# Performance work log

Measured on AMD Instinct MI355X. Metric: run time of the kernel, lower is better.

The kernel has to match this reference:

```python
import jax, jax.numpy as jnp
import numpy as np

B, T, H = 2, 2048, 2048
QH, KH, D = 16, 8, 128
F = 8192
EPS = 1e-06
MASK_VALUE = -1e30


def _rms_norm(x, gamma, eps=EPS):
    rms = jnp.sqrt(jnp.mean(x.astype(jnp.float32) ** 2, axis=-1, keepdims=True) + eps)
    return (gamma * x / rms).astype(jnp.bfloat16)


def _rope(x, sin, cos):
    # x: [B,T,h,D]; sin/cos: [B,T,D//2]
    x1, x2 = x[..., : x.shape[-1] // 2], x[..., x.shape[-1] // 2:]
    s, c = sin[:, :, None, :], cos[:, :, None, :]
    return jnp.concatenate([x1 * c - x2 * s, x2 * c + x1 * s], axis=-1)


def _attention(q, k, v, q_idx, k_idx, q_pos, k_pos):
    # q: [B,QH,T,D]; k,v: [B,KH,T,D]. Online-softmax tiling in the original is
    # mathematically identical to a single stable softmax over the full causal row.
    orig = q.dtype
    q = q.astype(jnp.float32)
    k = k.astype(jnp.float32)
    v = v.astype(jnp.float32)
    rep = q.shape[1] // k.shape[1]
    k = jnp.repeat(k, rep, axis=1)
    v = jnp.repeat(v, rep, axis=1)
    scale = 1.0 / jnp.sqrt(jnp.asarray(q.shape[-1], jnp.float32))
    s = jnp.einsum('bhqd,bhkd->bhqk', q, k) * scale
    mask = (q_idx[:, None, :, None] & k_idx[:, None, None, :]) & (
        q_pos[:, None, :, None] >= k_pos[:, None, None, :])
    s = jnp.where(mask, s, MASK_VALUE)
    p = jax.nn.softmax(s, axis=-1)
    o = jnp.einsum('bhqk,bhkd->bhqd', p, v)
    return o.astype(orig)


def _block(x, sin, cos, token_mask, pre_gamma, wq, wk, wv, q_gamma, k_gamma, wo,
           post_gamma, wg, wu, wd):
    bf = jnp.bfloat16
    Bx, Tx = x.shape[0], x.shape[1]
    x_norm = _rms_norm(x, pre_gamma)                     # bf16
    q = (x_norm @ wq.astype(bf)).reshape(Bx, Tx, QH, D)
    k = (x_norm @ wk.astype(bf)).reshape(Bx, Tx, KH, D)
    v = (x_norm @ wv.astype(bf)).reshape(Bx, Tx, KH, D)
    q = _rope(_rms_norm(q, q_gamma), sin, cos)           # promotes to f32 (matches flax)
    k = _rope(_rms_norm(k, k_gamma), sin, cos)
    idx = token_mask != 0
    pos = jax.lax.broadcasted_iota(jnp.int32, token_mask.shape, 1)
    attn = _attention(q.swapaxes(1, 2), k.swapaxes(1, 2), v.swapaxes(1, 2),
                      idx, idx, pos, pos)
    attn = attn.swapaxes(1, 2).reshape(Bx, Tx, QH * D)
    x = x + attn.astype(bf) @ wo.astype(bf)
    x_norm = _rms_norm(x, post_gamma)
    g = jax.nn.silu(x_norm @ wg.astype(bf))
    y = g * (x_norm @ wu.astype(bf))
    x = x + y @ wd.astype(bf)
    return x, k, v


def setup_inputs() -> dict:
    key = jax.random.key(0)
    ks = jax.random.split(key, 8)

    def w(kk, shape):
        return jax.random.normal(kk, shape, jnp.float32) * 0.02

    x = jax.random.normal(ks[0], (B, T, H), jnp.float32)
    pos = jnp.arange(T, dtype=jnp.float32)
    inv_freq = 1.0 / (10000.0 ** (jnp.arange(D // 2, dtype=jnp.float32) / (D // 2)))
    ang = pos[:, None] * inv_freq[None, :]
    sin = jnp.broadcast_to(jnp.sin(ang)[None], (B, T, D // 2))
    cos = jnp.broadcast_to(jnp.cos(ang)[None], (B, T, D // 2))
    return {
        'x': x, 'sin': sin, 'cos': cos,
        'token_mask': jnp.ones((B, T), jnp.int32),
        'layer_id': 0,
        'pre_gamma': jnp.ones((H,), jnp.float32),
        'wq': w(ks[1], (H, QH * D)),
        'wk': w(ks[2], (H, KH * D)),
        'wv': w(ks[3], (H, KH * D)),
        'q_gamma': jnp.ones((D,), jnp.float32),
        'k_gamma': jnp.ones((D,), jnp.float32),
        'wo': w(ks[4], (QH * D, H)),
        'post_gamma': jnp.ones((H,), jnp.float32),
        'wg': w(ks[5], (H, F)),
        'wu': w(ks[6], (H, F)),
        'wd': w(ks[7], (F, H)),
    }


def reference(x, sin, cos, token_mask, layer_id, pre_gamma, wq, wk, wv, q_gamma,
              k_gamma, wo, post_gamma, wg, wu, wd):
    # cache=None path: layer_id is unused.
    return _block(x, sin, cos, token_mask, pre_gamma, wq, wk, wv, q_gamma,
                  k_gamma, wo, post_gamma, wg, wu, wd)
```

## Files before the change

kernel.cpp:

```cpp
#include <hip/hip_runtime.h>
#include <hip/hip_bf16.h>


#define Bc  2
#define Tc  2048
#define Hc  2048
#define QHc 16
#define KHc 8
#define Dc  128
#define Fc  8192
#define Mc  (Bc*Tc)
#define FCHUNK 2048
#define EPSc 1e-6f
#define MASKVAL (-1e30f)

typedef __bf16  bf16x8 __attribute__((ext_vector_type(8)));
typedef short   short8 __attribute__((ext_vector_type(8)));
typedef float   f32x4  __attribute__((ext_vector_type(4)));

__device__ __forceinline__ float waveReduceSum(float v) {
    for (int off = 32; off > 0; off >>= 1) v += __shfl_down(v, off, 64);
    return v;
}

__device__ __forceinline__ void load_lds_16(const __hip_bfloat16* g,
                                            __hip_bfloat16* l) {
    __builtin_amdgcn_global_load_lds(
        (const __attribute__((address_space(1))) void*)g,
        (__attribute__((address_space(3))) void*)l, 16, 0, 0);
}

__global__ __launch_bounds__(256) void rmsnorm_f32_kernel(
    const float* __restrict__ in, const float* __restrict__ gamma,
    __hip_bfloat16* __restrict__ out, int width)
{
    const int row = blockIdx.x;
    const float* r = in + (size_t)row * width;
    float ss = 0.f;
    for (int i = threadIdx.x; i < width; i += 256) { float v = r[i]; ss += v * v; }
    ss = waveReduceSum(ss);
    __shared__ float red[4];
    if ((threadIdx.x & 63) == 0) red[threadIdx.x >> 6] = ss;
    __syncthreads();
    const float tot = red[0] + red[1] + red[2] + red[3];
    const float inv = 1.0f / sqrtf(tot / (float)width + EPSc);
    __hip_bfloat16* o = out + (size_t)row * width;
    for (int i = threadIdx.x; i < width; i += 256)
        o[i] = __float2bfloat16(gamma[i] * r[i] * inv);
}

__global__ __launch_bounds__(128) void qknorm_rope_kernel(
    const __hip_bfloat16* in, const float* __restrict__ gamma,
    const float* __restrict__ sinp, const float* __restrict__ cosp,
    __hip_bfloat16* outB, float* outF, int heads)
{
    const int row = blockIdx.x;
    const int bt  = row / heads;
    const int d   = threadIdx.x;
    const float v = __bfloat162float(in[(size_t)row * Dc + d]);
    float ss = waveReduceSum(v * v);
    __shared__ float red[2];
    __shared__ float nrm[Dc];
    if ((d & 63) == 0) red[d >> 6] = ss;
    __syncthreads();
    const float rms = sqrtf((red[0] + red[1]) * (1.0f / (float)Dc) + EPSc);
    const float xn = __bfloat162float(__float2bfloat16(gamma[d] * v / rms));
    nrm[d] = xn;
    __syncthreads();
    float res;
    if (d < 64) {
        const float s = sinp[(size_t)bt * 64 + d];
        const float c = cosp[(size_t)bt * 64 + d];
        res = nrm[d] * c - nrm[d + 64] * s;
    } else {
        const float s = sinp[(size_t)bt * 64 + (d - 64)];
        const float c = cosp[(size_t)bt * 64 + (d - 64)];
        res = nrm[d] * c + nrm[d - 64] * s;
    }
    outB[(size_t)row * Dc + d] = __float2bfloat16(res);
    if (outF) outF[(size_t)row * Dc + d] = res;
}

__global__ __launch_bounds__(256) void convert_transpose_kernel(
    const float* __restrict__ W, __hip_bfloat16* __restrict__ Wt, int K, int N)
{
    __shared__ float tile[32][33];
    const int tx = threadIdx.x & 31;
    const int ty = threadIdx.x >> 5;
    const int n0 = blockIdx.x * 32;
    const int k0 = blockIdx.y * 32;
    for (int r = 0; r < 4; ++r) {
        const int k = ty + r * 8;
        tile[k][tx] = W[(size_t)(k0 + k) * N + n0 + tx];
    }
    __syncthreads();
    for (int r = 0; r < 4; ++r) {
        const int n = ty + r * 8;
        Wt[(size_t)(n0 + n) * K + k0 + tx] = __float2bfloat16(tile[tx][n]);
    }
}


__device__ __forceinline__ void stage_unitA256(
    const __hip_bfloat16* __restrict__ Ag, __hip_bfloat16* bufBase,
    int m0, int lda, int kk0, int h, int tid)
{
#pragma unroll
    for (int p = 0; p < 2; ++p) {
        const int ci = p * 512 + tid;
        const int rl = ci >> 3;
        const int cc = ci & 7;
        const int grow = m0 + ((rl >> 6) * 128) + h * 64 + (rl & 63);
        const int scc = cc ^ (rl & 7);
        load_lds_16(Ag + (size_t)grow * lda + kk0 + scc * 8,
                    bufBase + h * 8192 + ci * 8);
    }
}

__device__ __forceinline__ void stage_unitB256(
    const __hip_bfloat16* __restrict__ Bg, __hip_bfloat16* bufBase,
    int n0, int ldt, int kk0, int h, int tid)
{
#pragma unroll
    for (int p = 0; p < 2; ++p) {
        const int ci = p * 512 + tid;
        const int rl = ci >> 3;
        const int cc = ci & 7;
        const int grow = n0 + h * 128 + rl;
        const int scc = cc ^ (rl & 7);
        load_lds_16(Bg + (size_t)grow * ldt + kk0 + scc * 8,
                    bufBase + h * 8192 + ci * 8);
    }
}

__device__ __forceinline__ bf16x8 read_frag256(const __hip_bfloat16* buf,
                                               int r, int w)
{
    const int cc = w ^ (r & 7);
    return *reinterpret_cast<const bf16x8*>(buf + r * 64 + cc * 8);
}

template <int MODE>
__global__ __launch_bounds__(512, 2) void gemm256_kernel(
    const __hip_bfloat16* __restrict__ A, const __hip_bfloat16* __restrict__ Bt,
    __hip_bfloat16* outB, float* outF, const float* resid,
    const __hip_bfloat16* gmul, int M, int N, int K, int lda, int ldt, int ldc)
{
    __shared__ __hip_bfloat16 smem[65536];
    __hip_bfloat16* Ab0 = smem;
    __hip_bfloat16* Ab1 = smem + 16384;
    __hip_bfloat16* Bb0 = smem + 32768;
    __hip_bfloat16* Bb1 = smem + 49152;

    const int tid  = threadIdx.x;
    const int lane = tid & 63;
    const int wave = tid >> 6;
    const int l15  = lane & 15;
    const int quad = lane >> 4;
    const int wm   = wave >> 2;
    const int wn   = wave & 3;
    const int m0   = blockIdx.y * 256;
    const int n0   = blockIdx.x * 256;
    const int NTt  = K >> 6;

    f32x4 acc[8][4];
    const f32x4 zero = {0.f, 0.f, 0.f, 0.f};
#pragma unroll
    for (int i = 0; i < 8; ++i)
#pragma unroll
        for (int j = 0; j < 4; ++j) acc[i][j] = zero;

    stage_unitA256(A, Ab0, m0, lda, 0, 0, tid);
    stage_unitA256(A, Ab0, m0, lda, 0, 1, tid);
    stage_unitB256(Bt, Bb0, n0, ldt, 0, 0, tid);
    stage_unitB256(Bt, Bb0, n0, ldt, 0, 1, tid);
    if (NTt > 1) {
        stage_unitA256(A, Ab1, m0, lda, 64, 0, tid);
        stage_unitB256(Bt, Bb1, n0, ldt, 64, 0, tid);
        stage_unitB256(Bt, Bb1, n0, ldt, 64, 1, tid);
    }
    asm volatile("s_waitcnt vmcnt(0)" ::: "memory");
    asm volatile("s_barrier" ::: "memory");

    bf16x8 bfr[4][2];
    bf16x8 af[4];

#define GB_READ_B(BB)                                                         \
    _Pragma("unroll")                                                         \
    for (int nt = 0; nt < 4; ++nt) {                                          \
        bfr[nt][0] = read_frag256(BB, wn * 64 + nt * 16 + l15, quad);         \
        bfr[nt][1] = read_frag256(BB, wn * 64 + nt * 16 + l15, 4 + quad);     \
    }
#define GB_READ_A(AB, MG, KS)                                                 \
    _Pragma("unroll")                                                         \
    for (int mq = 0; mq < 4; ++mq)                                            \
        af[mq] = read_frag256(AB, (MG)*128 + wm * 64 + mq * 16 + l15,         \
                              (KS)*4 + quad);
#define GB_MFMA(MG, KS)                                                       \
    __builtin_amdgcn_s_setprio(1);                                            \
    _Pragma("unroll")                                                         \
    for (int nt = 0; nt < 4; ++nt)                                            \
    _Pragma("unroll")                                                         \
    for (int mq = 0; mq < 4; ++mq)                                            \
        acc[(MG)*4 + mq][nt] = __builtin_amdgcn_mfma_f32_16x16x32_bf16(       \
            af[mq], bfr[nt][KS], acc[(MG)*4 + mq][nt], 0, 0, 0);              \
    __builtin_amdgcn_s_setprio(0);
#define SBAR256 asm volatile("s_barrier" ::: "memory")
#define VMC6    asm volatile("s_waitcnt vmcnt(6)" ::: "memory")

    const int nIter = NTt >> 1;
    for (int it = 0; it < nIter; ++it) {
        const int t1 = 2 * it + 1, t2 = 2 * it + 2, t3 = 2 * it + 3;
        GB_READ_B(Bb0); GB_READ_A(Ab0, 0, 0);
        stage_unitA256(A, Ab1, m0, lda, t1 * 64, 1, tid);
        SBAR256; GB_MFMA(0, 0); SBAR256;
        GB_READ_A(Ab0, 0, 1);
        if (t2 < NTt) stage_unitB256(Bt, Bb0, n0, ldt, t2 * 64, 0, tid);
        SBAR256; GB_MFMA(0, 1); SBAR256;
        GB_READ_A(Ab0, 1, 0);
        if (t2 < NTt) stage_unitB256(Bt, Bb0, n0, ldt, t2 * 64, 1, tid);
        SBAR256; GB_MFMA(1, 0); SBAR256;
        GB_READ_A(Ab0, 1, 1);
        if (t2 < NTt) stage_unitA256(A, Ab0, m0, lda, t2 * 64, 0, tid);
        SBAR256; GB_MFMA(1, 1); VMC6; SBAR256;
        GB_READ_B(Bb1); GB_READ_A(Ab1, 0, 0);
        if (t2 < NTt) stage_unitA256(A, Ab0, m0, lda, t2 * 64, 1, tid);
        SBAR256; GB_MFMA(0, 0); SBAR256;
        GB_READ_A(Ab1, 0, 1);
        if (t3 < NTt) stage_unitB256(Bt, Bb1, n0, ldt, t3 * 64, 0, tid);
        SBAR256; GB_MFMA(0, 1); SBAR256;
        GB_READ_A(Ab1, 1, 0);
        if (t3 < NTt) stage_unitB256(Bt, Bb1, n0, ldt, t3 * 64, 1, tid);
        SBAR256; GB_MFMA(1, 0); SBAR256;
        GB_READ_A(Ab1, 1, 1);
        if (t3 < NTt) stage_unitA256(A, Ab1, m0, lda, t3 * 64, 0, tid);
        SBAR256; GB_MFMA(1, 1); VMC6; SBAR256;
    }

#undef GB_READ_B
#undef GB_READ_A
#undef GB_MFMA
#undef SBAR256
#undef VMC6

#pragma unroll
    for (int m = 0; m < 8; ++m) {
#pragma unroll
        for (int nt = 0; nt < 4; ++nt) {
            const f32x4 a  = acc[m][nt];
            const int col  = n0 + wn * 64 + nt * 16 + l15;
            const int rowb = m0 + wm * 128 + (m >> 2) * 64 + (m & 3) * 16 + quad * 4;
#pragma unroll
            for (int r = 0; r < 4; ++r) {
                const size_t idx = (size_t)(rowb + r) * ldc + col;
                const float val = a[r];
                if constexpr (MODE == 0) {
                    outB[idx] = __float2bfloat16(val);
                } else if constexpr (MODE == 1) {
                    outF[idx] = resid[idx] +
                                __bfloat162float(__float2bfloat16(val));
                } else if constexpr (MODE == 3) {
                    const float g = __bfloat162float(gmul[idx]);
                    const float sil = __bfloat162float(
                        __float2bfloat16(g / (1.f + __expf(-g))));
                    const float u = __bfloat162float(__float2bfloat16(val));
                    outB[idx] = __float2bfloat16(sil * u);
                } else {
                    const __hip_bfloat16 b = __float2bfloat16(val);
                    outB[idx] = b;
                    outF[idx] = __bfloat162float(b);
                }
            }
        }
    }
}

template <int MODE>
__global__ __launch_bounds__(256) void gemm_bt_kernel(
    const __hip_bfloat16* __restrict__ A, const __hip_bfloat16* __restrict__ Bt,
    __hip_bfloat16* outB, float* outF, const float* resid,
    const __hip_bfloat16* gmul, int M, int N, int K, int lda, int ldt)
{
    __shared__ __hip_bfloat16 As[128 * 32];
    __shared__ __hip_bfloat16 Bs[128 * 32];

    const int tid  = threadIdx.x;
    const int lane = tid & 63;
    const int wave = tid >> 6;
    const int l15  = lane & 15;
    const int quad = lane >> 4;
    const int q8   = quad * 8;
    const int wm   = wave >> 1;
    const int wn   = wave & 1;
    const int m0   = blockIdx.y * 128;
    const int n0   = blockIdx.x * 128;

    const int c0 = tid, c1 = tid + 256;
    const int r0 = c0 >> 2, o0 = (c0 & 3) * 8;
    const int r1 = c1 >> 2, o1 = (c1 & 3) * 8;
    const __hip_bfloat16* gA0 = A + (size_t)(m0 + r0) * lda + o0;
    const __hip_bfloat16* gA1 = A + (size_t)(m0 + r1) * lda + o1;
    const __hip_bfloat16* gB0 = Bt + (size_t)(n0 + r0) * ldt + o0;
    const __hip_bfloat16* gB1 = Bt + (size_t)(n0 + r1) * ldt + o1;

    f32x4 acc[4][4];
    const f32x4 zero = {0.f, 0.f, 0.f, 0.f};
#pragma unroll
    for (int i = 0; i < 4; ++i)
#pragma unroll
        for (int j = 0; j < 4; ++j) acc[i][j] = zero;

    for (int k0 = 0; k0 < K; k0 += 32) {
        __syncthreads();
        load_lds_16(gA0 + k0, As + c0 * 8);
        load_lds_16(gA1 + k0, As + c1 * 8);
        load_lds_16(gB0 + k0, Bs + c0 * 8);
        load_lds_16(gB1 + k0, Bs + c1 * 8);
        __syncthreads();

        bf16x8 af[4], bfv[4];
#pragma unroll
        for (int mt = 0; mt < 4; ++mt)
            af[mt] = *reinterpret_cast<const bf16x8*>(
                As + (wm * 64 + mt * 16 + l15) * 32 + q8);
#pragma unroll
        for (int nt = 0; nt < 4; ++nt)
            bfv[nt] = *reinterpret_cast<const bf16x8*>(
                Bs + (wn * 64 + nt * 16 + l15) * 32 + q8);
#pragma unroll
        for (int mt = 0; mt < 4; ++mt)
#pragma unroll
            for (int nt = 0; nt < 4; ++nt)
                acc[mt][nt] = __builtin_amdgcn_mfma_f32_16x16x32_bf16(
                    af[mt], bfv[nt], acc[mt][nt], 0, 0, 0);
    }

#pragma unroll
    for (int mt = 0; mt < 4; ++mt) {
#pragma unroll
        for (int nt = 0; nt < 4; ++nt) {
            const f32x4 a  = acc[mt][nt];
            const int col  = n0 + wn * 64 + nt * 16 + l15;
            const int rowb = m0 + wm * 64 + mt * 16 + quad * 4;
#pragma unroll
            for (int r = 0; r < 4; ++r) {
                const size_t idx = (size_t)(rowb + r) * N + col;
                const float val = a[r];
                if constexpr (MODE == 0) {
                    outB[idx] = __float2bfloat16(val);
                } else if constexpr (MODE == 1) {
                    outF[idx] = resid[idx] +
                                __bfloat162float(__float2bfloat16(val));
                } else if constexpr (MODE == 3) {
                    const float g = __bfloat162float(gmul[idx]);
                    const float sil = __bfloat162float(
                        __float2bfloat16(g / (1.f + __expf(-g))));
                    const float u = __bfloat162float(__float2bfloat16(val));
                    outB[idx] = __float2bfloat16(sil * u);
                } else {
                    const __hip_bfloat16 b = __float2bfloat16(val);
                    outB[idx] = b;
                    outF[idx] = __bfloat162float(b);
                }
            }
        }
    }
}

template <int MODE>
__global__ __launch_bounds__(256) void gemm_kernel(
    const __hip_bfloat16* __restrict__ A, const float* __restrict__ Bw,
    __hip_bfloat16* outB, float* outF, const float* resid,
    const __hip_bfloat16* gmul, int M, int N, int K, int ldb)
{
    __shared__ __hip_bfloat16 As[128][32];
    __shared__ __hip_bfloat16 Bs[128][40];

    const int tid  = threadIdx.x;
    const int lane = tid & 63;
    const int wave = tid >> 6;
    const int l15  = lane & 15;
    const int quad = lane >> 4;
    const int q8   = quad * 8;
    const int wm   = wave >> 1;
    const int wn   = wave & 1;
    const int m0   = blockIdx.y * 128;
    const int n0   = blockIdx.x * 128;

    f32x4 acc[4][4];
    const f32x4 zero = {0.f, 0.f, 0.f, 0.f};
#pragma unroll
    for (int i = 0; i < 4; ++i)
#pragma unroll
        for (int j = 0; j < 4; ++j) acc[i][j] = zero;

    const int nK = K >> 5;
    for (int kt = 0; kt < nK; ++kt) {
        const int k0 = kt << 5;
        __syncthreads();
#pragma unroll
        for (int vv = 0; vv < 2; ++vv) {
            const int vi  = vv * 256 + tid;
            const int row = vi >> 2;
            const int col = (vi & 3) * 8;
            *(short8*)(&As[row][col]) =
                *(const short8*)(A + (size_t)(m0 + row) * K + k0 + col);
        }
        {
            const int n  = tid & 127;
            const int kk = tid >> 7;
            const float* bp = Bw + (size_t)k0 * ldb + n0 + n;
#pragma unroll
            for (int p = 0; p < 16; ++p) {
                const int k = p * 2 + kk;
                Bs[n][k] = __float2bfloat16(bp[(size_t)k * ldb]);
            }
        }
        __syncthreads();
        bf16x8 af[4], bfv[4];
#pragma unroll
        for (int mt = 0; mt < 4; ++mt)
            af[mt] = *reinterpret_cast<const bf16x8*>(&As[wm * 64 + mt * 16 + l15][q8]);
#pragma unroll
        for (int nt = 0; nt < 4; ++nt)
            bfv[nt] = *reinterpret_cast<const bf16x8*>(&Bs[wn * 64 + nt * 16 + l15][q8]);
#pragma unroll
        for (int mt = 0; mt < 4; ++mt)
#pragma unroll
            for (int nt = 0; nt < 4; ++nt)
                acc[mt][nt] = __builtin_amdgcn_mfma_f32_16x16x32_bf16(
                    af[mt], bfv[nt], acc[mt][nt], 0, 0, 0);
    }

#pragma unroll
    for (int mt = 0; mt < 4; ++mt) {
#pragma unroll
        for (int nt = 0; nt < 4; ++nt) {
            const f32x4 a  = acc[mt][nt];
            const int col  = n0 + wn * 64 + nt * 16 + l15;
            const int rowb = m0 + wm * 64 + mt * 16 + quad * 4;
#pragma unroll
            for (int r = 0; r < 4; ++r) {
                const size_t idx = (size_t)(rowb + r) * N + col;
                const float val = a[r];
                if constexpr (MODE == 0) {
                    outB[idx] = __float2bfloat16(val);
                } else if constexpr (MODE == 1) {
                    outF[idx] = resid[idx] +
                                __bfloat162float(__float2bfloat16(val));
                } else if constexpr (MODE == 3) {
                    const float g = __bfloat162float(gmul[idx]);
                    const float sil = __bfloat162float(
                        __float2bfloat16(g / (1.f + __expf(-g))));
                    const float u = __bfloat162float(__float2bfloat16(val));
                    outB[idx] = __float2bfloat16(sil * u);
                } else {
                    const __hip_bfloat16 b = __float2bfloat16(val);
                    outB[idx] = b;
                    outF[idx] = __bfloat162float(b);
                }
            }
        }
    }
}

__global__ __launch_bounds__(256) void flash_attn_kernel(
    const __hip_bfloat16* q, const __hip_bfloat16* __restrict__ k,
    const __hip_bfloat16* __restrict__ v, const int* __restrict__ mask,
    __hip_bfloat16* out)
{
    __shared__ unsigned short Ks[64][136];
    __shared__ unsigned short Vs[128][72];
    __shared__ unsigned short Ps[4][16][72];
    __shared__ int msk[64];

    const int tid  = threadIdx.x;
    const int lane = tid & 63;
    const int wave = tid >> 6;
    const int l15  = lane & 15;
    const int quad = lane >> 4;
    const int q0   = blockIdx.x * 64;
    const int bh   = blockIdx.y;
    const int b    = bh >> 4;
    const int h    = bh & 15;
    const int kh   = h >> 1;

    const float scale = 0.08838834764831845f;

    bf16x8 qf[4];
    {
        const __hip_bfloat16* qp =
            q + (((size_t)(b * Tc + q0 + wave * 16 + l15)) * QHc + h) * Dc;
#pragma unroll
        for (int kk = 0; kk < 4; ++kk)
            qf[kk] = *(const bf16x8*)(qp + kk * 32 + quad * 8);
    }

    float mrow[4] = {MASKVAL, MASKVAL, MASKVAL, MASKVAL};
    float lrow[4] = {0.f, 0.f, 0.f, 0.f};
    f32x4 oacc[8];
#pragma unroll
    for (int i = 0; i < 8; ++i) oacc[i] = (f32x4){0.f, 0.f, 0.f, 0.f};

    const int ktmax = q0 >> 6;
    for (int kt = 0; kt <= ktmax; ++kt) {
        const int kvbase = kt * 64;
        __syncthreads();
#pragma unroll
        for (int i = 0; i < 4; ++i) {
            const int c  = i * 256 + tid;
            const int kv = c >> 4;
            const int d0 = (c & 15) * 8;
            *(bf16x8*)(&Ks[kv][d0]) = *(const bf16x8*)(
                k + (((size_t)(b * Tc + kvbase + kv)) * KHc + kh) * Dc + d0);
        }
        {
            const int kv = tid & 63;
            const int g0 = (tid >> 6) * 4;
            for (int g = g0; g < g0 + 4; ++g) {
                const int d0 = g * 8;
                const short8 tmp = *(const short8*)(
                    v + (((size_t)(b * Tc + kvbase + kv)) * KHc + kh) * Dc + d0);
#pragma unroll
                for (int j = 0; j < 8; ++j)
                    Vs[d0 + j][kv] = (unsigned short)tmp[j];
            }
        }
        if (tid < 64) msk[tid] = mask[b * Tc + kvbase + tid];
        __syncthreads();

        f32x4 sacc[4];
#pragma unroll
        for (int nt = 0; nt < 4; ++nt) sacc[nt] = (f32x4){0.f, 0.f, 0.f, 0.f};
#pragma unroll
        for (int nt = 0; nt < 4; ++nt)
#pragma unroll
            for (int kk = 0; kk < 4; ++kk) {
                const bf16x8 kf = *(const bf16x8*)(&Ks[nt * 16 + l15][kk * 32 + quad * 8]);
                sacc[nt] = __builtin_amdgcn_mfma_f32_16x16x32_bf16(
                    qf[kk], kf, sacc[nt], 0, 0, 0);
            }

        float tmax[4] = {MASKVAL, MASKVAL, MASKVAL, MASKVAL};
#pragma unroll
        for (int nt = 0; nt < 4; ++nt) {
            const int kvpos  = kvbase + nt * 16 + l15;
            const bool kvld  = (msk[nt * 16 + l15] != 0);
#pragma unroll
            for (int r = 0; r < 4; ++r) {
                const int qr = q0 + wave * 16 + quad * 4 + r;
                float s = sacc[nt][r] * scale;
                s = (kvld && kvpos <= qr) ? s : MASKVAL;
                sacc[nt][r] = s;
                tmax[r] = fmaxf(tmax[r], s);
            }
        }
#pragma unroll
        for (int r = 0; r < 4; ++r)
            for (int off = 1; off < 16; off <<= 1)
                tmax[r] = fmaxf(tmax[r], __shfl_xor(tmax[r], off, 64));

        float alpha[4];
#pragma unroll
        for (int r = 0; r < 4; ++r) {
            const float mnew = fmaxf(mrow[r], tmax[r]);
            alpha[r] = __expf(mrow[r] - mnew);
            mrow[r]  = mnew;
        }
        float tsum[4] = {0.f, 0.f, 0.f, 0.f};
#pragma unroll
        for (int nt = 0; nt < 4; ++nt)
#pragma unroll
            for (int r = 0; r < 4; ++r) {
                const float p = __expf(sacc[nt][r] - mrow[r]);
                sacc[nt][r] = p;
                tsum[r] += p;
            }
#pragma unroll
        for (int r = 0; r < 4; ++r)
            for (int off = 1; off < 16; off <<= 1)
                tsum[r] += __shfl_xor(tsum[r], off, 64);
#pragma unroll
        for (int r = 0; r < 4; ++r)
            lrow[r] = lrow[r] * alpha[r] + tsum[r];

#pragma unroll
        for (int nt = 0; nt < 4; ++nt)
#pragma unroll
            for (int r = 0; r < 4; ++r) {
                const __hip_bfloat16 pb = __float2bfloat16(sacc[nt][r]);
                Ps[wave][quad * 4 + r][nt * 16 + l15] =
                    *(const unsigned short*)&pb;
            }
        __syncthreads();

#pragma unroll
        for (int ntd = 0; ntd < 8; ++ntd)
#pragma unroll
            for (int r = 0; r < 4; ++r) oacc[ntd][r] *= alpha[r];
        bf16x8 pa[2];
#pragma unroll
        for (int kk2 = 0; kk2 < 2; ++kk2)
            pa[kk2] = *(const bf16x8*)(&Ps[wave][l15][kk2 * 32 + quad * 8]);
#pragma unroll
        for (int ntd = 0; ntd < 8; ++ntd)
#pragma unroll
            for (int kk2 = 0; kk2 < 2; ++kk2) {
                const bf16x8 vf = *(const bf16x8*)(
                    &Vs[ntd * 16 + l15][kk2 * 32 + quad * 8]);
                oacc[ntd] = __builtin_amdgcn_mfma_f32_16x16x32_bf16(
                    pa[kk2], vf, oacc[ntd], 0, 0, 0);
            }
    }

#pragma unroll
    for (int ntd = 0; ntd < 8; ++ntd)
#pragma unroll
        for (int r = 0; r < 4; ++r) {
            const float li = lrow[r];
            const float o  = (li > 0.f) ? oacc[ntd][r] / li : 0.f;
            const int qr   = q0 + wave * 16 + quad * 4 + r;
            out[(((size_t)(b * Tc + qr)) * QHc + h) * Dc + ntd * 16 + l15] =
                __float2bfloat16(o);
        }
}

extern "C" void kernel_launch(void* const* d_in, const int* in_sizes, int n_in,
                              void* d_out, int out_size, void* d_ws, size_t ws_size,
                              hipStream_t stream) {
    const float* x          = (const float*)d_in[0];
    const float* sinp       = (const float*)d_in[1];
    const float* cosp       = (const float*)d_in[2];
    const int*   token_mask = (const int*)d_in[3];
    const float* pre_gamma  = (const float*)d_in[5];
    const float* wq         = (const float*)d_in[6];
    const float* wk         = (const float*)d_in[7];
    const float* wv         = (const float*)d_in[8];
    const float* q_gamma    = (const float*)d_in[9];
    const float* k_gamma    = (const float*)d_in[10];
    const float* wo         = (const float*)d_in[11];
    const float* post_gamma = (const float*)d_in[12];
    const float* wg         = (const float*)d_in[13];
    const float* wu         = (const float*)d_in[14];
    const float* wd         = (const float*)d_in[15];

    float* outx = (float*)d_out;
    float* outk = outx + (size_t)Bc * Tc * Hc;
    float* outv = outk + (size_t)Bc * Tc * KHc * Dc;

    const bool fast = (ws_size >= 176160768ull);

    if (fast) {
        char* w = (char*)d_ws;
        __hip_bfloat16* wq_t  = (__hip_bfloat16*)(w);
        __hip_bfloat16* wk_t  = (__hip_bfloat16*)(w + 8388608);
        __hip_bfloat16* wv_t  = (__hip_bfloat16*)(w + 12582912);
        __hip_bfloat16* wo_t  = (__hip_bfloat16*)(w + 16777216);
        __hip_bfloat16* wg_t  = (__hip_bfloat16*)(w + 25165824);
        __hip_bfloat16* wu_t  = (__hip_bfloat16*)(w + 58720256);
        __hip_bfloat16* wd_t  = (__hip_bfloat16*)(w + 92274688);
        __hip_bfloat16* xnorm = (__hip_bfloat16*)(w + 125829120);
        __hip_bfloat16* qbuf  = (__hip_bfloat16*)(w + 142606336);
        __hip_bfloat16* kbuf  = (__hip_bfloat16*)(w + 159383552);
        __hip_bfloat16* vbuf  = (__hip_bfloat16*)(w + 167772160);
        __hip_bfloat16* Gbig  = qbuf;

        convert_transpose_kernel<<<dim3(Hc/32, Hc/32), 256, 0, stream>>>(wq, wq_t, Hc, Hc);
        convert_transpose_kernel<<<dim3((KHc*Dc)/32, Hc/32), 256, 0, stream>>>(wk, wk_t, Hc, KHc*Dc);
        convert_transpose_kernel<<<dim3((KHc*Dc)/32, Hc/32), 256, 0, stream>>>(wv, wv_t, Hc, KHc*Dc);
        convert_transpose_kernel<<<dim3(Hc/32, Hc/32), 256, 0, stream>>>(wo, wo_t, Hc, Hc);
        convert_transpose_kernel<<<dim3(Fc/32, Hc/32), 256, 0, stream>>>(wg, wg_t, Hc, Fc);
        convert_transpose_kernel<<<dim3(Fc/32, Hc/32), 256, 0, stream>>>(wu, wu_t, Hc, Fc);
        convert_transpose_kernel<<<dim3(Hc/32, Fc/32), 256, 0, stream>>>(wd, wd_t, Fc, Hc);

        rmsnorm_f32_kernel<<<Mc, 256, 0, stream>>>(x, pre_gamma, xnorm, Hc);

        gemm256_kernel<0><<<dim3(Hc/256, Mc/256), 512, 0, stream>>>(
            xnorm, wq_t, qbuf, nullptr, nullptr, nullptr, Mc, Hc, Hc, Hc, Hc, Hc);
        gemm_bt_kernel<0><<<dim3((KHc*Dc)/128, Mc/128), 256, 0, stream>>>(
            xnorm, wk_t, kbuf, nullptr, nullptr, nullptr, Mc, KHc*Dc, Hc, Hc, Hc);
        gemm_bt_kernel<4><<<dim3((KHc*Dc)/128, Mc/128), 256, 0, stream>>>(
            xnorm, wv_t, vbuf, outv, nullptr, nullptr, Mc, KHc*Dc, Hc, Hc, Hc);

        qknorm_rope_kernel<<<Mc*QHc, 128, 0, stream>>>(
            qbuf, q_gamma, sinp, cosp, qbuf, nullptr, QHc);
        qknorm_rope_kernel<<<Mc*KHc, 128, 0, stream>>>(
            kbuf, k_gamma, sinp, cosp, kbuf, outk, KHc);

        flash_attn_kernel<<<dim3(Tc/64, Bc*QHc), 256, 0, stream>>>(
            qbuf, kbuf, vbuf, token_mask, qbuf);

        gemm256_kernel<1><<<dim3(Hc/256, Mc/256), 512, 0, stream>>>(
            qbuf, wo_t, nullptr, outx, x, nullptr, Mc, Hc, Hc, Hc, Hc, Hc);

        rmsnorm_f32_kernel<<<Mc, 256, 0, stream>>>(outx, post_gamma, xnorm, Hc);

        for (int hh = 0; hh < 2; ++hh) {
            const __hip_bfloat16* wg_h = wg_t + (size_t)hh * 4096 * Hc;
            const __hip_bfloat16* wu_h = wu_t + (size_t)hh * 4096 * Hc;
            const __hip_bfloat16* wd_h = wd_t + (size_t)hh * 4096;
            gemm256_kernel<0><<<dim3(4096/256, Mc/256), 512, 0, stream>>>(
                xnorm, wg_h, Gbig, nullptr, nullptr, nullptr,
                Mc, 4096, Hc, Hc, Hc, 4096);
            gemm256_kernel<3><<<dim3(4096/256, Mc/256), 512, 0, stream>>>(
                xnorm, wu_h, Gbig, nullptr, nullptr, Gbig,
                Mc, 4096, Hc, Hc, Hc, 4096);
            gemm256_kernel<1><<<dim3(Hc/256, Mc/256), 512, 0, stream>>>(
                Gbig, wd_h, nullptr, outx, outx, nullptr,
                Mc, Hc, 4096, 4096, Fc, Hc);
        }
    } else {
        char* w = (char*)d_ws;
        __hip_bfloat16* xnorm = (__hip_bfloat16*)(w);
        __hip_bfloat16* qbuf  = (__hip_bfloat16*)(w + 16777216);
        __hip_bfloat16* kbuf  = (__hip_bfloat16*)(w + 33554432);
        __hip_bfloat16* vbuf  = (__hip_bfloat16*)(w + 41943040);
        __hip_bfloat16* Gtmp  = qbuf;

        rmsnorm_f32_kernel<<<Mc, 256, 0, stream>>>(x, pre_gamma, xnorm, Hc);
        gemm_kernel<0><<<dim3(Hc/128, Mc/128), 256, 0, stream>>>(
            xnorm, wq, qbuf, nullptr, nullptr, nullptr, Mc, Hc, Hc, Hc);
        gemm_kernel<0><<<dim3((KHc*Dc)/128, Mc/128), 256, 0, stream>>>(
            xnorm, wk, kbuf, nullptr, nullptr, nullptr, Mc, KHc*Dc, Hc, KHc*Dc);
        gemm_kernel<4><<<dim3((KHc*Dc)/128, Mc/128), 256, 0, stream>>>(
            xnorm, wv, vbuf, outv, nullptr, nullptr, Mc, KHc*Dc, Hc, KHc*Dc);
        qknorm_rope_kernel<<<Mc*QHc, 128, 0, stream>>>(
            qbuf, q_gamma, sinp, cosp, qbuf, nullptr, QHc);
        qknorm_rope_kernel<<<Mc*KHc, 128, 0, stream>>>(
            kbuf, k_gamma, sinp, cosp, kbuf, outk, KHc);
        flash_attn_kernel<<<dim3(Tc/64, Bc*QHc), 256, 0, stream>>>(
            qbuf, kbuf, vbuf, token_mask, qbuf);
        gemm_kernel<1><<<dim3(Hc/128, Mc/128), 256, 0, stream>>>(
            qbuf, wo, nullptr, outx, x, nullptr, Mc, Hc, Hc, Hc);
        rmsnorm_f32_kernel<<<Mc, 256, 0, stream>>>(outx, post_gamma, xnorm, Hc);
        for (int c = 0; c < 4; ++c) {
            const float* wg_c = wg + (size_t)c * FCHUNK;
            const float* wu_c = wu + (size_t)c * FCHUNK;
            const float* wd_c = wd + (size_t)c * FCHUNK * Hc;
            gemm_kernel<0><<<dim3(FCHUNK/128, Mc/128), 256, 0, stream>>>(
                xnorm, wg_c, Gtmp, nullptr, nullptr, nullptr, Mc, FCHUNK, Hc, Fc);
            gemm_kernel<3><<<dim3(FCHUNK/128, Mc/128), 256, 0, stream>>>(
                xnorm, wu_c, Gtmp, nullptr, nullptr, Gtmp, Mc, FCHUNK, Hc, Fc);
            gemm_kernel<1><<<dim3(Hc/128, Mc/128), 256, 0, stream>>>(
                Gtmp, wd_c, nullptr, outx, outx, nullptr, Mc, Hc, FCHUNK, Hc);
        }
    }
}
```

Before: 1.381 ms.

## Fuse QKV projection, split-K down-proj with atomics, balance and prefetch flash attention

The Q, K and V projections become one 256-tile GEMM over a concatenated weight, with output routing by column range, replacing three launches. The FFN down projection uses split-K over two z-slices and accumulates into the residual with float atomics, so the two slices run in parallel. Flash attention gives each block a long and a short causal tile to balance work, register-prefetches the next K/V tile, drops one barrier and raises wave priority around the MFMAs. Atomics make the summation order nondeterministic, and the fused QKV path assumes wq_t, wk_t and wv_t are contiguous.

```diff
diff --git a/kernel.cpp b/kernel.cpp
--- a/kernel.cpp
+++ b/kernel.cpp
@@ -151,6 +151,11 @@
     __hip_bfloat16* Ab1 = smem + 16384;
     __hip_bfloat16* Bb0 = smem + 32768;
     __hip_bfloat16* Bb1 = smem + 49152;
+
+    if constexpr (MODE == 2) {
+        A  += (size_t)blockIdx.z * K;
+        Bt += (size_t)blockIdx.z * K;
+    }
 
     const int tid  = threadIdx.x;
     const int lane = tid & 63;
@@ -259,16 +264,31 @@
                 } else if constexpr (MODE == 1) {
                     outF[idx] = resid[idx] +
                                 __bfloat162float(__float2bfloat16(val));
+                } else if constexpr (MODE == 2) {
+                    unsafeAtomicAdd(&outF[idx], val);
                 } else if constexpr (MODE == 3) {
                     const float g = __bfloat162float(gmul[idx]);
                     const float sil = __bfloat162float(
                         __float2bfloat16(g / (1.f + __expf(-g))));
                     const float u = __bfloat162float(__float2bfloat16(val));
                     outB[idx] = __float2bfloat16(sil * u);
-                } else {
+                } else if constexpr (MODE == 4) {
                     const __hip_bfloat16 b = __float2bfloat16(val);
                     outB[idx] = b;
                     outF[idx] = __bfloat162float(b);
+                } else {
+                    if (n0 < 2048) {
+                        outB[(size_t)(rowb + r) * 2048 + col] =
+                            __float2bfloat16(val);
+                    } else if (n0 < 3072) {
+                        outB[8388608 + (size_t)(rowb + r) * 1024 + (col - 2048)] =
+                            __float2bfloat16(val);
+                    } else {
+                        const __hip_bfloat16 b = __float2bfloat16(val);
+                        outB[12582912 + (size_t)(rowb + r) * 1024 + (col - 3072)] = b;
+                        outF[(size_t)(rowb + r) * 1024 + (col - 3072)] =
+                            __bfloat162float(b);
+                    }
                 }
             }
         }
@@ -276,13 +296,13 @@
 }
 
 template <int MODE>
-__global__ __launch_bounds__(256) void gemm_bt_kernel(
-    const __hip_bfloat16* __restrict__ A, const __hip_bfloat16* __restrict__ Bt,
+__global__ __launch_bounds__(256) void gemm_kernel(
+    const __hip_bfloat16* __restrict__ A, const float* __restrict__ Bw,
     __hip_bfloat16* outB, float* outF, const float* resid,
-    const __hip_bfloat16* gmul, int M, int N, int K, int lda, int ldt)
-{
-    __shared__ __hip_bfloat16 As[128 * 32];
-    __shared__ __hip_bfloat16 Bs[128 * 32];
+    const __hip_bfloat16* gmul, int M, int N, int K, int ldb)
+{
+    __shared__ __hip_bfloat16 As[128][32];
+    __shared__ __hip_bfloat16 Bs[128][40];
 
     const int tid  = threadIdx.x;
     const int lane = tid & 63;
@@ -295,14 +315,6 @@
     const int m0   = blockIdx.y * 128;
     const int n0   = blockIdx.x * 128;
 
-    const int c0 = tid, c1 = tid + 256;
-    const int r0 = c0 >> 2, o0 = (c0 & 3) * 8;
-    const int r1 = c1 >> 2, o1 = (c1 & 3) * 8;
-    const __hip_bfloat16* gA0 = A + (size_t)(m0 + r0) * lda + o0;
-    const __hip_bfloat16* gA1 = A + (size_t)(m0 + r1) * lda + o1;
-    const __hip_bfloat16* gB0 = Bt + (size_t)(n0 + r0) * ldt + o0;
-    const __hip_bfloat16* gB1 = Bt + (size_t)(n0 + r1) * ldt + o1;
-
     f32x4 acc[4][4];
     const f32x4 zero = {0.f, 0.f, 0.f, 0.f};
 #pragma unroll
@@ -310,23 +322,36 @@
 #pragma unroll
         for (int j = 0; j < 4; ++j) acc[i][j] = zero;
 
-    for (int k0 = 0; k0 < K; k0 += 32) {
+    const int nK = K >> 5;
+    for (int kt = 0; kt < nK; ++kt) {
+        const int k0 = kt << 5;
         __syncthreads();
-        load_lds_16(gA0 + k0, As + c0 * 8);
-        load_lds_16(gA1 + k0, As + c1 * 8);
-        load_lds_16(gB0 + k0, Bs + c0 * 8);
-        load_lds_16(gB1 + k0, Bs + c1 * 8);
+#pragma unroll
+        for (int vv = 0; vv < 2; ++vv) {
+            const int vi  = vv * 256 + tid;
+            const int row = vi >> 2;
+            const int col = (vi & 3) * 8;
+            *(short8*)(&As[row][col]) =
+                *(const short8*)(A + (size_t)(m0 + row) * K + k0 + col);
+        }
+        {
+            const int n  = tid & 127;
+            const int kk = tid >> 7;
+            const float* bp = Bw + (size_t)k0 * ldb + n0 + n;
+#pragma unroll
+            for (int p = 0; p < 16; ++p) {
+                const int k = p * 2 + kk;
+                Bs[n][k] = __float2bfloat16(bp[(size_t)k * ldb]);
+            }
+        }
         __syncthreads();
-
         bf16x8 af[4], bfv[4];
 #pragma unroll
         for (int mt = 0; mt < 4; ++mt)
-            af[mt] = *reinterpret_cast<const bf16x8*>(
-                As + (wm * 64 + mt * 16 + l15) * 32 + q8);
+            af[mt] = *reinterpret_cast<const bf16x8*>(&As[wm * 64 + mt * 16 + l15][q8]);
 #pragma unroll
         for (int nt = 0; nt < 4; ++nt)
-            bfv[nt] = *reinterpret_cast<const bf16x8*>(
-                Bs + (wn * 64 + nt * 16 + l15) * 32 + q8);
+            bfv[nt] = *reinterpret_cast<const bf16x8*>(&Bs[wn * 64 + nt * 16 + l15][q8]);
 #pragma unroll
         for (int mt = 0; mt < 4; ++mt)
 #pragma unroll
@@ -367,262 +392,192 @@
     }
 }
 
-template <int MODE>
-__global__ __launch_bounds__(256) void gemm_kernel(
-    const __hip_bfloat16* __restrict__ A, const float* __restrict__ Bw,
-    __hip_bfloat16* outB, float* outF, const float* resid,
-    const __hip_bfloat16* gmul, int M, int N, int K, int ldb)
-{
-    __shared__ __hip_bfloat16 As[128][32];
-    __shared__ __hip_bfloat16 Bs[128][40];
+__global__ __launch_bounds__(256) void flash_attn_kernel(
+    const __hip_bfloat16* q, const __hip_bfloat16* __restrict__ k,
+    const __hip_bfloat16* __restrict__ v, const int* __restrict__ mask,
+    __hip_bfloat16* out)
+{
+    __shared__ unsigned short Ks[64][136];
+    __shared__ unsigned short Vs[128][72];
+    __shared__ unsigned short Ps[4][16][72];
+    __shared__ int msk[64];
 
     const int tid  = threadIdx.x;
     const int lane = tid & 63;
     const int wave = tid >> 6;
     const int l15  = lane & 15;
     const int quad = lane >> 4;
-    const int q8   = quad * 8;
-    const int wm   = wave >> 1;
-    const int wn   = wave & 1;
-    const int m0   = blockIdx.y * 128;
-    const int n0   = blockIdx.x * 128;
-
-    f32x4 acc[4][4];
-    const f32x4 zero = {0.f, 0.f, 0.f, 0.f};
-#pragma unroll
-    for (int i = 0; i < 4; ++i)
-#pragma unroll
-        for (int j = 0; j < 4; ++j) acc[i][j] = zero;
-
-    const int nK = K >> 5;
-    for (int kt = 0; kt < nK; ++kt) {
-        const int k0 = kt << 5;
-        __syncthreads();
-#pragma unroll
-        for (int vv = 0; vv < 2; ++vv) {
-            const int vi  = vv * 256 + tid;
-            const int row = vi >> 2;
-            const int col = (vi & 3) * 8;
-            *(short8*)(&As[row][col]) =
-                *(const short8*)(A + (size_t)(m0 + row) * K + k0 + col);
-        }
-        {
-            const int n  = tid & 127;
-            const int kk = tid >> 7;
-            const float* bp = Bw + (size_t)k0 * ldb + n0 + n;
-#pragma unroll
-            for (int p = 0; p < 16; ++p) {
-                const int k = p * 2 + kk;
-                Bs[n][k] = __float2bfloat16(bp[(size_t)k * ldb]);
-            }
-        }
-        __syncthreads();
-        bf16x8 af[4], bfv[4];
-#pragma unroll
-        for (int mt = 0; mt < 4; ++mt)
-            af[mt] = *reinterpret_cast<const bf16x8*>(&As[wm * 64 + mt * 16 + l15][q8]);
-#pragma unroll
-        for (int nt = 0; nt < 4; ++nt)
-            bfv[nt] = *reinterpret_cast<const bf16x8*>(&Bs[wn * 64 + nt * 16 + l15][q8]);
-#pragma unroll
-        for (int mt = 0; mt < 4; ++mt)
-#pragma unroll
-            for (int nt = 0; nt < 4; ++nt)
-                acc[mt][nt] = __builtin_amdgcn_mfma_f32_16x16x32_bf16(
-                    af[mt], bfv[nt], acc[mt][nt], 0, 0, 0);
-    }
-
-#pragma unroll
-    for (int mt = 0; mt < 4; ++mt) {
-#pragma unroll
-        for (int nt = 0; nt < 4; ++nt) {
-            const f32x4 a  = acc[mt][nt];
-            const int col  = n0 + wn * 64 + nt * 16 + l15;
-            const int rowb = m0 + wm * 64 + mt * 16 + quad * 4;
-#pragma unroll
-            for (int r = 0; r < 4; ++r) {
-                const size_t idx = (size_t)(rowb + r) * N + col;
-                const float val = a[r];
-                if constexpr (MODE == 0) {
-                    outB[idx] = __float2bfloat16(val);
-                } else if constexpr (MODE == 1) {
-                    outF[idx] = resid[idx] +
-                                __bfloat162float(__float2bfloat16(val));
-                } else if constexpr (MODE == 3) {
-                    const float g = __bfloat162float(gmul[idx]);
-                    const float sil = __bfloat162float(
-                        __float2bfloat16(g / (1.f + __expf(-g))));
-                    const float u = __bfloat162float(__float2bfloat16(val));
-                    outB[idx] = __float2bfloat16(sil * u);
-                } else {
-                    const __hip_bfloat16 b = __float2bfloat16(val);
-                    outB[idx] = b;
-                    outF[idx] = __bfloat162float(b);
-                }
-            }
-        }
-    }
-}
-
-__global__ __launch_bounds__(256) void flash_attn_kernel(
-    const __hip_bfloat16* q, const __hip_bfloat16* __restrict__ k,
-    const __hip_bfloat16* __restrict__ v, const int* __restrict__ mask,
-    __hip_bfloat16* out)
-{
-    __shared__ unsigned short Ks[64][136];
-    __shared__ unsigned short Vs[128][72];
-    __shared__ unsigned short Ps[4][16][72];
-    __shared__ int msk[64];
-
-    const int tid  = threadIdx.x;
-    const int lane = tid & 63;
-    const int wave = tid >> 6;
-    const int l15  = lane & 15;
-    const int quad = lane >> 4;
-    const int q0   = blockIdx.x * 64;
     const int bh   = blockIdx.y;
     const int b    = bh >> 4;
     const int h    = bh & 15;
     const int kh   = h >> 1;
-
     const float scale = 0.08838834764831845f;
 
-    bf16x8 qf[4];
-    {
-        const __hip_bfloat16* qp =
-            q + (((size_t)(b * Tc + q0 + wave * 16 + l15)) * QHc + h) * Dc;
-#pragma unroll
-        for (int kk = 0; kk < 4; ++kk)
-            qf[kk] = *(const bf16x8*)(qp + kk * 32 + quad * 8);
-    }
-
-    float mrow[4] = {MASKVAL, MASKVAL, MASKVAL, MASKVAL};
-    float lrow[4] = {0.f, 0.f, 0.f, 0.f};
-    f32x4 oacc[8];
-#pragma unroll
-    for (int i = 0; i < 8; ++i) oacc[i] = (f32x4){0.f, 0.f, 0.f, 0.f};
-
-    const int ktmax = q0 >> 6;
-    for (int kt = 0; kt <= ktmax; ++kt) {
-        const int kvbase = kt * 64;
-        __syncthreads();
-#pragma unroll
-        for (int i = 0; i < 4; ++i) {
-            const int c  = i * 256 + tid;
-            const int kv = c >> 4;
-            const int d0 = (c & 15) * 8;
-            *(bf16x8*)(&Ks[kv][d0]) = *(const bf16x8*)(
-                k + (((size_t)(b * Tc + kvbase + kv)) * KHc + kh) * Dc + d0);
-        }
+    const int skv = tid >> 4;
+    const int sd0 = (tid & 15) * 8;
+    const int vkv = tid & 63;
+    const int vg0 = (tid >> 6) * 4;
+
+    for (int half = 0; half < 2; ++half) {
+        const int qt = (half == 0) ? (31 - (int)blockIdx.x) : (int)blockIdx.x;
+        const int q0 = qt * 64;
+
+        bf16x8 qf[4];
         {
-            const int kv = tid & 63;
-            const int g0 = (tid >> 6) * 4;
-            for (int g = g0; g < g0 + 4; ++g) {
-                const int d0 = g * 8;
-                const short8 tmp = *(const short8*)(
-                    v + (((size_t)(b * Tc + kvbase + kv)) * KHc + kh) * Dc + d0);
+            const __hip_bfloat16* qp =
+                q + (((size_t)(b * Tc + q0 + wave * 16 + l15)) * QHc + h) * Dc;
+#pragma unroll
+            for (int kk = 0; kk < 4; ++kk)
+                qf[kk] = *(const bf16x8*)(qp + kk * 32 + quad * 8);
+        }
+
+        float mrow[4] = {MASKVAL, MASKVAL, MASKVAL, MASKVAL};
+        float lrow[4] = {0.f, 0.f, 0.f, 0.f};
+        f32x4 oacc[8];
+#pragma unroll
+        for (int i = 0; i < 8; ++i) oacc[i] = (f32x4){0.f, 0.f, 0.f, 0.f};
+
+        bf16x8 kreg[4];
+        short8 vreg[4];
+        int mreg = 0;
+#pragma unroll
+        for (int i = 0; i < 4; ++i)
+            kreg[i] = *(const bf16x8*)(
+                k + (((size_t)(b * Tc + skv + i * 16)) * KHc + kh) * Dc + sd0);
+#pragma unroll
+        for (int g = 0; g < 4; ++g)
+            vreg[g] = *(const short8*)(
+                v + (((size_t)(b * Tc + vkv)) * KHc + kh) * Dc + (vg0 + g) * 8);
+        if (tid < 64) mreg = mask[b * Tc + tid];
+
+        const int ktmax = qt;
+        for (int kt = 0; kt <= ktmax; ++kt) {
+            const int kvbase = kt * 64;
+            __syncthreads();
+#pragma unroll
+            for (int i = 0; i < 4; ++i)
+                *(bf16x8*)(&Ks[skv + i * 16][sd0]) = kreg[i];
+#pragma unroll
+            for (int g = 0; g < 4; ++g) {
+                const int d0 = (vg0 + g) * 8;
 #pragma unroll
                 for (int j = 0; j < 8; ++j)
-                    Vs[d0 + j][kv] = (unsigned short)tmp[j];
-            }
-        }
-        if (tid < 64) msk[tid] = mask[b * Tc + kvbase + tid];
-        __syncthreads();
-
-        f32x4 sacc[4];
-#pragma unroll
-        for (int nt = 0; nt < 4; ++nt) sacc[nt] = (f32x4){0.f, 0.f, 0.f, 0.f};
-#pragma unroll
-        for (int nt = 0; nt < 4; ++nt)
-#pragma unroll
-            for (int kk = 0; kk < 4; ++kk) {
-                const bf16x8 kf = *(const bf16x8*)(&Ks[nt * 16 + l15][kk * 32 + quad * 8]);
-                sacc[nt] = __builtin_amdgcn_mfma_f32_16x16x32_bf16(
-                    qf[kk], kf, sacc[nt], 0, 0, 0);
-            }
-
-        float tmax[4] = {MASKVAL, MASKVAL, MASKVAL, MASKVAL};
-#pragma unroll
-        for (int nt = 0; nt < 4; ++nt) {
-            const int kvpos  = kvbase + nt * 16 + l15;
-            const bool kvld  = (msk[nt * 16 + l15] != 0);
+                    Vs[d0 + j][vkv] = (unsigned short)vreg[g][j];
+            }
+            if (tid < 64) msk[tid] = mreg;
+            __syncthreads();
+
+            if (kt < ktmax) {
+                const int nb = (kt + 1) * 64;
+#pragma unroll
+                for (int i = 0; i < 4; ++i)
+                    kreg[i] = *(const bf16x8*)(
+                        k + (((size_t)(b * Tc + nb + skv + i * 16)) * KHc + kh) * Dc + sd0);
+#pragma unroll
+                for (int g = 0; g < 4; ++g)
+                    vreg[g] = *(const short8*)(
+                        v + (((size_t)(b * Tc + nb + vkv)) * KHc + kh) * Dc + (vg0 + g) * 8);
+                if (tid < 64) mreg = mask[b * Tc + nb + tid];
+            }
+
+            f32x4 sacc[4];
+#pragma unroll
+            for (int nt = 0; nt < 4; ++nt) sacc[nt] = (f32x4){0.f, 0.f, 0.f, 0.f};
+            __builtin_amdgcn_s_setprio(1);
+#pragma unroll
+            for (int nt = 0; nt < 4; ++nt)
+#pragma unroll
+                for (int kk = 0; kk < 4; ++kk) {
+                    const bf16x8 kf = *(const bf16x8*)(&Ks[nt * 16 + l15][kk * 32 + quad * 8]);
+                    sacc[nt] = __builtin_amdgcn_mfma_f32_16x16x32_bf16(
+                        qf[kk], kf, sacc[nt], 0, 0, 0);
+                }
+            __builtin_amdgcn_s_setprio(0);
+
+            float tmax[4] = {MASKVAL, MASKVAL, MASKVAL, MASKVAL};
+#pragma unroll
+            for (int nt = 0; nt < 4; ++nt) {
+                const int kvpos  = kvbase + nt * 16 + l15;
+                const bool kvld  = (msk[nt * 16 + l15] != 0);
+#pragma unroll
+                for (int r = 0; r < 4; ++r) {
+                    const int qr = q0 + wave * 16 + quad * 4 + r;
+                    float s = sacc[nt][r] * scale;
+                    s = (kvld && kvpos <= qr) ? s : MASKVAL;
+                    sacc[nt][r] = s;
+                    tmax[r] = fmaxf(tmax[r], s);
+                }
+            }
+#pragma unroll
+            for (int r = 0; r < 4; ++r)
+                for (int off = 1; off < 16; off <<= 1)
+                    tmax[r] = fmaxf(tmax[r], __shfl_xor(tmax[r], off, 64));
+
+            float alpha[4];
 #pragma unroll
             for (int r = 0; r < 4; ++r) {
-                const int qr = q0 + wave * 16 + quad * 4 + r;
-                float s = sacc[nt][r] * scale;
-                s = (kvld && kvpos <= qr) ? s : MASKVAL;
-                sacc[nt][r] = s;
-                tmax[r] = fmaxf(tmax[r], s);
-            }
-        }
-#pragma unroll
-        for (int r = 0; r < 4; ++r)
-            for (int off = 1; off < 16; off <<= 1)
-                tmax[r] = fmaxf(tmax[r], __shfl_xor(tmax[r], off, 64));
-
-        float alpha[4];
-#pragma unroll
-        for (int r = 0; r < 4; ++r) {
-            const float mnew = fmaxf(mrow[r], tmax[r]);
-            alpha[r] = __expf(mrow[r] - mnew);
-            mrow[r]  = mnew;
-        }
-        float tsum[4] = {0.f, 0.f, 0.f, 0.f};
-#pragma unroll
-        for (int nt = 0; nt < 4; ++nt)
+                const float mnew = fmaxf(mrow[r], tmax[r]);
+                alpha[r] = __expf(mrow[r] - mnew);
+                mrow[r]  = mnew;
+            }
+            float tsum[4] = {0.f, 0.f, 0.f, 0.f};
+#pragma unroll
+            for (int nt = 0; nt < 4; ++nt)
+#pragma unroll
+                for (int r = 0; r < 4; ++r) {
+                    const float p = __expf(sacc[nt][r] - mrow[r]);
+                    sacc[nt][r] = p;
+                    tsum[r] += p;
+                }
+#pragma unroll
+            for (int r = 0; r < 4; ++r)
+                for (int off = 1; off < 16; off <<= 1)
+                    tsum[r] += __shfl_xor(tsum[r], off, 64);
+#pragma unroll
+            for (int r = 0; r < 4; ++r)
+                lrow[r] = lrow[r] * alpha[r] + tsum[r];
+
+#pragma unroll
+            for (int nt = 0; nt < 4; ++nt)
+#pragma unroll
+                for (int r = 0; r < 4; ++r) {
+                    const __hip_bfloat16 pb = __float2bfloat16(sacc[nt][r]);
+                    Ps[wave][quad * 4 + r][nt * 16 + l15] =
+                        *(const unsigned short*)&pb;
+                }
+
+#pragma unroll
+            for (int ntd = 0; ntd < 8; ++ntd)
+#pragma unroll
+                for (int r = 0; r < 4; ++r) oacc[ntd][r] *= alpha[r];
+            bf16x8 pa[2];
+#pragma unroll
+            for (int kk2 = 0; kk2 < 2; ++kk2)
+                pa[kk2] = *(const bf16x8*)(&Ps[wave][l15][kk2 * 32 + quad * 8]);
+            __builtin_amdgcn_s_setprio(1);
+#pragma unroll
+            for (int ntd = 0; ntd < 8; ++ntd)
+#pragma unroll
+                for (int kk2 = 0; kk2 < 2; ++kk2) {
+                    const bf16x8 vf = *(const bf16x8*)(
+                        &Vs[ntd * 16 + l15][kk2 * 32 + quad * 8]);
+                    oacc[ntd] = __builtin_amdgcn_mfma_f32_16x16x32_bf16(
+                        pa[kk2], vf, oacc[ntd], 0, 0, 0);
+                }
+            __builtin_amdgcn_s_setprio(0);
+        }
+
+#pragma unroll
+        for (int ntd = 0; ntd < 8; ++ntd)
 #pragma unroll
             for (int r = 0; r < 4; ++r) {
-                const float p = __expf(sacc[nt][r] - mrow[r]);
-                sacc[nt][r] = p;
-                tsum[r] += p;
-            }
-#pragma unroll
-        for (int r = 0; r < 4; ++r)
-            for (int off = 1; off < 16; off <<= 1)
-                tsum[r] += __shfl_xor(tsum[r], off, 64);
-#pragma unroll
-        for (int r = 0; r < 4; ++r)
-            lrow[r] = lrow[r] * alpha[r] + tsum[r];
-
-#pragma unroll
-        for (int nt = 0; nt < 4; ++nt)
-#pragma unroll
-            for (int r = 0; r < 4; ++r) {
-                const __hip_bfloat16 pb = __float2bfloat16(sacc[nt][r]);
-                Ps[wave][quad * 4 + r][nt * 16 + l15] =
-                    *(const unsigned short*)&pb;
-            }
-        __syncthreads();
-
-#pragma unroll
-        for (int ntd = 0; ntd < 8; ++ntd)
-#pragma unroll
-            for (int r = 0; r < 4; ++r) oacc[ntd][r] *= alpha[r];
-        bf16x8 pa[2];
-#pragma unroll
-        for (int kk2 = 0; kk2 < 2; ++kk2)
-            pa[kk2] = *(const bf16x8*)(&Ps[wave][l15][kk2 * 32 + quad * 8]);
-#pragma unroll
-        for (int ntd = 0; ntd < 8; ++ntd)
-#pragma unroll
-            for (int kk2 = 0; kk2 < 2; ++kk2) {
-                const bf16x8 vf = *(const bf16x8*)(
-                    &Vs[ntd * 16 + l15][kk2 * 32 + quad * 8]);
-                oacc[ntd] = __builtin_amdgcn_mfma_f32_16x16x32_bf16(
-                    pa[kk2], vf, oacc[ntd], 0, 0, 0);
-            }
-    }
-
-#pragma unroll
-    for (int ntd = 0; ntd < 8; ++ntd)
-#pragma unroll
-        for (int r = 0; r < 4; ++r) {
-            const float li = lrow[r];
-            const float o  = (li > 0.f) ? oacc[ntd][r] / li : 0.f;
-            const int qr   = q0 + wave * 16 + quad * 4 + r;
-            out[(((size_t)(b * Tc + qr)) * QHc + h) * Dc + ntd * 16 + l15] =
-                __float2bfloat16(o);
-        }
+                const float li = lrow[r];
+                const float o  = (li > 0.f) ? oacc[ntd][r] / li : 0.f;
+                const int qr   = q0 + wave * 16 + quad * 4 + r;
+                out[(((size_t)(b * Tc + qr)) * QHc + h) * Dc + ntd * 16 + l15] =
+                    __float2bfloat16(o);
+            }
+    }
 }
 
 extern "C" void kernel_launch(void* const* d_in, const int* in_sizes, int n_in,
@@ -675,19 +630,15 @@
 
         rmsnorm_f32_kernel<<<Mc, 256, 0, stream>>>(x, pre_gamma, xnorm, Hc);
 
-        gemm256_kernel<0><<<dim3(Hc/256, Mc/256), 512, 0, stream>>>(
-            xnorm, wq_t, qbuf, nullptr, nullptr, nullptr, Mc, Hc, Hc, Hc, Hc, Hc);
-        gemm_bt_kernel<0><<<dim3((KHc*Dc)/128, Mc/128), 256, 0, stream>>>(
-            xnorm, wk_t, kbuf, nullptr, nullptr, nullptr, Mc, KHc*Dc, Hc, Hc, Hc);
-        gemm_bt_kernel<4><<<dim3((KHc*Dc)/128, Mc/128), 256, 0, stream>>>(
-            xnorm, wv_t, vbuf, outv, nullptr, nullptr, Mc, KHc*Dc, Hc, Hc, Hc);
+        gemm256_kernel<5><<<dim3(4096/256, Mc/256), 512, 0, stream>>>(
+            xnorm, wq_t, qbuf, outv, nullptr, nullptr, Mc, 4096, Hc, Hc, Hc, 0);
 
         qknorm_rope_kernel<<<Mc*QHc, 128, 0, stream>>>(
             qbuf, q_gamma, sinp, cosp, qbuf, nullptr, QHc);
         qknorm_rope_kernel<<<Mc*KHc, 128, 0, stream>>>(
             kbuf, k_gamma, sinp, cosp, kbuf, outk, KHc);
 
-        flash_attn_kernel<<<dim3(Tc/64, Bc*QHc), 256, 0, stream>>>(
+        flash_attn_kernel<<<dim3(Tc/128, Bc*QHc), 256, 0, stream>>>(
             qbuf, kbuf, vbuf, token_mask, qbuf);
 
         gemm256_kernel<1><<<dim3(Hc/256, Mc/256), 512, 0, stream>>>(
@@ -705,9 +656,9 @@
             gemm256_kernel<3><<<dim3(4096/256, Mc/256), 512, 0, stream>>>(
                 xnorm, wu_h, Gbig, nullptr, nullptr, Gbig,
                 Mc, 4096, Hc, Hc, Hc, 4096);
-            gemm256_kernel<1><<<dim3(Hc/256, Mc/256), 512, 0, stream>>>(
-                Gbig, wd_h, nullptr, outx, outx, nullptr,
-                Mc, Hc, 4096, 4096, Fc, Hc);
+            gemm256_kernel<2><<<dim3(Hc/256, Mc/256, 2), 512, 0, stream>>>(
+                Gbig, wd_h, nullptr, outx, nullptr, nullptr,
+                Mc, Hc, 2048, 4096, Fc, Hc);
         }
     } else {
         char* w = (char*)d_ws;
@@ -728,7 +679,7 @@
             qbuf, q_gamma, sinp, cosp, qbuf, nullptr, QHc);
         qknorm_rope_kernel<<<Mc*KHc, 128, 0, stream>>>(
             kbuf, k_gamma, sinp, cosp, kbuf, outk, KHc);
-        flash_attn_kernel<<<dim3(Tc/64, Bc*QHc), 256, 0, stream>>>(
+        flash_attn_kernel<<<dim3(Tc/128, Bc*QHc), 256, 0, stream>>>(
             qbuf, kbuf, vbuf, token_mask, qbuf);
         gemm_kernel<1><<<dim3(Hc/128, Mc/128), 256, 0, stream>>>(
             qbuf, wo, nullptr, outx, x, nullptr, Mc, Hc, Hc, Hc);
```

Result: faster. 1.165 ms (-15.6%).
